# Performance work log

Hardware: AMD Instinct MI355X
Metric: run time of the kernel (lower is better)

Reference implementation:

```python
import jax, jax.numpy as jnp
import numpy as np
from jax import lax

WIN = 9  # NCC window per axis (default [9]*3)

# 3x3x3 edge/shape kernels, shape [O=1, I=1, 3, 3, 3]
_LAP = np.zeros((3, 3, 3), np.float32)
_LAP[1, 1, 1] = 6.0
_LAP[0, 1, 1] = _LAP[2, 1, 1] = -1.0
_LAP[1, 0, 1] = _LAP[1, 2, 1] = -1.0
_LAP[1, 1, 0] = _LAP[1, 1, 2] = -1.0
LAP_K = jnp.asarray(_LAP)[None, None]

_row = np.array([[-1.0, 0.0, 1.0], [-2.0, 0.0, 2.0], [-1.0, 0.0, 1.0]], np.float32)
SOBEL_X = jnp.asarray(np.stack([_row, _row, _row], axis=0))[None, None]
_plane = np.array([[-1.0, -2.0, -1.0], [-1.0, -2.0, -1.0], [-1.0, -2.0, -1.0]], np.float32)
SOBEL_Y = jnp.asarray(np.stack([_plane, np.zeros((3, 3), np.float32), -_plane], axis=0))[None, None]
_zp = np.array([[-1.0, -1.0, -1.0], [0.0, 0.0, 0.0], [1.0, 1.0, 1.0]], np.float32)
SOBEL_Z = jnp.asarray(np.stack([_zp, 2.0 * _zp, _zp], axis=0))[None, None]


def conv3d(x, k, pad):
    # x: [N,C,D,H,W], k: [O,I,kd,kh,kw]
    return lax.conv_general_dilated(x, k, (1, 1, 1), [(pad, pad)] * 3)


def box_sum(x, win=WIN):
    # Separable all-ones box filter == dense ones conv (same math, fewer FLOPs)
    pad = win // 2
    for axis in range(3):
        kshape = [1, 1, 1, 1, 1]
        kshape[2 + axis] = win
        k = jnp.ones(kshape, x.dtype)
        padding = [(pad, pad) if a == axis else (0, 0) for a in range(3)]
        x = lax.conv_general_dilated(x, k, (1, 1, 1), padding)
    return x


def ncc_vxm(Ii, Ji, win=WIN):
    win_size = float(win ** 3)
    I2, J2, IJ = Ii * Ii, Ji * Ji, Ii * Ji
    I_sum = box_sum(Ii, win)
    J_sum = box_sum(Ji, win)
    I2_sum = box_sum(I2, win)
    J2_sum = box_sum(J2, win)
    IJ_sum = box_sum(IJ, win)
    u_I = I_sum / win_size
    u_J = J_sum / win_size
    cross = IJ_sum - u_J * I_sum - u_I * J_sum + u_I * u_J * win_size
    I_var = I2_sum - 2.0 * u_I * I_sum + u_I * u_I * win_size
    J_var = J2_sum - 2.0 * u_J * J_sum + u_J * u_J * win_size
    cc = cross * cross / (I_var * J_var + 1e-5)
    return -jnp.mean(cc)


def edge_detection(v):
    return conv3d(v, LAP_K, pad=1)


def shape_detection(v):
    gx = conv3d(v, SOBEL_X, pad=1)
    gy = conv3d(v, SOBEL_Y, pad=1)
    gz = conv3d(v, SOBEL_Z, pad=1)
    return jnp.sqrt(gx * gx + gy * gy + gz * gz)


def setup_inputs() -> dict:
    key = jax.random.key(0)
    k1, k2 = jax.random.split(key)
    shape = (1, 1, 160, 192, 160)
    y_true = jax.random.uniform(k1, shape, dtype=jnp.float32)
    y_pred = jax.random.uniform(k2, shape, dtype=jnp.float32)
    return {"y_true": y_true, "y_pred": y_pred}


def reference(y_true, y_pred):
    loss_orig = ncc_vxm(y_true, y_pred)
    loss_edge = ncc_vxm(edge_detection(y_true), edge_detection(y_pred))
    loss_shape = ncc_vxm(shape_detection(y_true), shape_detection(y_pred))
    return 0.8 * loss_orig + 0.1 * loss_edge + 0.1 * loss_shape
```

## Files before the change

### kernel.cpp

```cpp
#include <hip/hip_runtime.h>
#include <hip/hip_fp16.h>
#include <math.h>

#define DD 160
#define HHH 192
#define WWW 160
constexpr int HW = HHH * WWW;
constexpr int NV = DD * HHH * WWW;
constexpr int W4 = WWW / 4;
constexpr int HC = 4;
constexpr int DC = 4;
constexpr int SC = 5;

constexpr int NB_WH  = (W4 * DD * (HHH / HC)) / 256;
constexpr int NB_SO  = (W4 * HHH * (DD / SC)) / 256;
constexpr int NB_LAP = (NV / 4) / 256;
constexpr int NB_DCC = (W4 * HHH * (DD / DC)) / 256;

__device__ __forceinline__ float4 ldg4(const float* __restrict__ p, int idx, bool ok) {
    float4 z = make_float4(0.f, 0.f, 0.f, 0.f);
    return ok ? *(const float4*)(p + idx) : z;
}

__device__ __forceinline__ void st_h4(__half* __restrict__ t, int idx,
                                      float s0, float s1, float s2, float s3) {
    union { __half2 h2[2]; uint2 u; } pk;
    pk.h2[0] = __floats2half2_rn(s0, s1);
    pk.h2[1] = __floats2half2_rn(s2, s3);
    *(uint2*)(t + idx) = pk.u;
}

__device__ __forceinline__ void ld_h4(const __half* __restrict__ t, int idx, float o[4]) {
    union { __half2 h2[2]; uint2 u; } pk;
    pk.u = *(const uint2*)(t + idx);
    o[0] = __low2float(pk.h2[0]); o[1] = __high2float(pk.h2[0]);
    o[2] = __low2float(pk.h2[1]); o[3] = __high2float(pk.h2[1]);
}

__device__ __forceinline__ void lap_body(int t, const float* __restrict__ a,
                                         const float* __restrict__ b,
                                         __half* __restrict__ oa, __half* __restrict__ ob) {
    int w = (t % W4) * 4;
    int h = (t / W4) % HHH;
    int d = t / (W4 * HHH);
    int idx = (d * HHH + h) * WWW + w;
    bool dok0 = d > 0, dok1 = d < DD - 1, hok0 = h > 0, hok1 = h < HHH - 1;
#pragma unroll
    for (int s = 0; s < 2; s++) {
        const float* p = s ? b : a;
        __half* o = s ? ob : oa;
        float4 c = *(const float4*)(p + idx);
        float m1 = (w > 0) ? p[idx - 1] : 0.f;
        float p4 = (w + 4 < WWW) ? p[idx + 4] : 0.f;
        float4 dm = ldg4(p, idx - HW, dok0);
        float4 dp = ldg4(p, idx + HW, dok1);
        float4 hm = ldg4(p, idx - WWW, hok0);
        float4 hp = ldg4(p, idx + WWW, hok1);
        st_h4(o, idx,
              6.f * c.x - (m1 + c.y + dm.x + dp.x + hm.x + hp.x),
              6.f * c.y - (c.x + c.z + dm.y + dp.y + hm.y + hp.y),
              6.f * c.z - (c.y + c.w + dm.z + dp.z + hm.z + hp.z),
              6.f * c.w - (c.z + p4 + dm.w + dp.w + hm.w + hp.w));
    }
}

__device__ __forceinline__ void sobel_slice(const float* __restrict__ p, int s, int h, int w,
                                            float a1[4], float a2[4], float a3[4]) {
#pragma unroll
    for (int k = 0; k < 4; k++) { a1[k] = 0.f; a2[k] = 0.f; a3[k] = 0.f; }
#pragma unroll
    for (int kh = -1; kh <= 1; kh++) {
        int h2 = h + kh;
        if ((unsigned)h2 < (unsigned)HHH) {
            int rb = (s * HHH + h2) * WWW + w;
            float4 cen = *(const float4*)(p + rb);
            float xm = (w > 0) ? p[rb - 1] : 0.f;
            float xp = (w + 4 < WWW) ? p[rb + 4] : 0.f;
            float xv[6] = {xm, cen.x, cen.y, cen.z, cen.w, xp};
            float smh = (kh == 0) ? 2.f : 1.f;
            float grh = (float)kh;
#pragma unroll
            for (int k = 0; k < 4; k++) {
                float gw = xv[k + 2] - xv[k];
                float pw = xv[k] + xv[k + 1] + xv[k + 2];
                float sw = pw + xv[k + 1];
                a1[k] += smh * gw;
                a2[k] += sw;
                a3[k] += grh * pw;
            }
        }
    }
}

__device__ __forceinline__ void sobel_body(int t, const float* __restrict__ a,
                                           const float* __restrict__ b,
                                           __half* __restrict__ oa, __half* __restrict__ ob) {
    int w = (t % W4) * 4;
    int h = (t / W4) % HHH;
    int c = t / (W4 * HHH);
    int d0 = c * SC;

    float A1[2][3][4], A2[2][3][4], A3[2][3][4];
#pragma unroll
    for (int r = 0; r < 2; r++)
#pragma unroll
        for (int j = 0; j < 3; j++)
#pragma unroll
            for (int k = 0; k < 4; k++) { A1[r][j][k] = 0.f; A2[r][j][k] = 0.f; A3[r][j][k] = 0.f; }

#pragma unroll
    for (int i = 0; i < SC + 2; i++) {
        int s = d0 - 1 + i;
#pragma unroll
        for (int r = 0; r < 2; r++)
#pragma unroll
            for (int k = 0; k < 4; k++) {
                A1[r][0][k] = A1[r][1][k]; A2[r][0][k] = A2[r][1][k]; A3[r][0][k] = A3[r][1][k];
                A1[r][1][k] = A1[r][2][k]; A2[r][1][k] = A2[r][2][k]; A3[r][1][k] = A3[r][2][k];
            }
        if (s >= 0 && s < DD) {
            sobel_slice(a, s, h, w, A1[0][2], A2[0][2], A3[0][2]);
            sobel_slice(b, s, h, w, A1[1][2], A2[1][2], A3[1][2]);
        } else {
#pragma unroll
            for (int r = 0; r < 2; r++)
#pragma unroll
                for (int k = 0; k < 4; k++) { A1[r][2][k] = 0.f; A2[r][2][k] = 0.f; A3[r][2][k] = 0.f; }
        }
        if (i >= 2) {
            int d = s - 1;
            int idx = (d * HHH + h) * WWW + w;
            float va[4], vb[4];
#pragma unroll
            for (int k = 0; k < 4; k++) {
                float gx = A1[0][0][k] + A1[0][1][k] + A1[0][2][k];
                float gy = A2[0][2][k] - A2[0][0][k];
                float gz = A3[0][0][k] + 2.f * A3[0][1][k] + A3[0][2][k];
                va[k] = sqrtf(gx * gx + gy * gy + gz * gz);
                gx = A1[1][0][k] + A1[1][1][k] + A1[1][2][k];
                gy = A2[1][2][k] - A2[1][0][k];
                gz = A3[1][0][k] + 2.f * A3[1][1][k] + A3[1][2][k];
                vb[k] = sqrtf(gx * gx + gy * gy + gz * gz);
            }
            st_h4(oa, idx, va[0], va[1], va[2], va[3]);
            st_h4(ob, idx, vb[0], vb[1], vb[2], vb[3]);
        }
    }
}

__device__ __forceinline__ void q5_from(const float x[12], const float y[12], float q[5][4]) {
    float s0 = 0, s1 = 0, s2 = 0, s3 = 0, s4 = 0;
#pragma unroll
    for (int j = 0; j < 9; j++) {
        s0 += x[j]; s1 += y[j];
        s2 += x[j] * x[j]; s3 += y[j] * y[j]; s4 += x[j] * y[j];
    }
    q[0][0] = s0; q[1][0] = s1; q[2][0] = s2; q[3][0] = s3; q[4][0] = s4;
#pragma unroll
    for (int k = 1; k < 4; k++) {
        q[0][k] = q[0][k - 1] + x[k + 8] - x[k - 1];
        q[1][k] = q[1][k - 1] + y[k + 8] - y[k - 1];
        q[2][k] = q[2][k - 1] + x[k + 8] * x[k + 8] - x[k - 1] * x[k - 1];
        q[3][k] = q[3][k - 1] + y[k + 8] * y[k + 8] - y[k - 1] * y[k - 1];
        q[4][k] = q[4][k - 1] + x[k + 8] * y[k + 8] - x[k - 1] * y[k - 1];
    }
}

__device__ __forceinline__ void ld12(const float* __restrict__ p, int rowbase, int w, float x[12]) {
    bool lo = (w >= 4);
    bool hi = (w + 7 < WWW);
    float4 x0 = ldg4(p, rowbase + w - 4, lo);
    float4 x1 = *(const float4*)(p + rowbase + w);
    float4 x2 = ldg4(p, rowbase + w + 4, hi);
    x[0] = x0.x; x[1] = x0.y; x[2] = x0.z; x[3] = x0.w;
    x[4] = x1.x; x[5] = x1.y; x[6] = x1.z; x[7] = x1.w;
    x[8] = x2.x; x[9] = x2.y; x[10] = x2.z; x[11] = x2.w;
}

__device__ __forceinline__ void ld12(const __half* __restrict__ p, int rowbase, int w, float x[12]) {
    bool lo = (w >= 4);
    bool hi = (w + 7 < WWW);
    union { __half2 h2[2]; uint2 u; } u0, u1, u2;
    uint2 z = make_uint2(0, 0);
    u0.u = lo ? *(const uint2*)(p + rowbase + w - 4) : z;
    u1.u = *(const uint2*)(p + rowbase + w);
    u2.u = hi ? *(const uint2*)(p + rowbase + w + 4) : z;
    x[0] = __low2float(u0.h2[0]); x[1] = __high2float(u0.h2[0]);
    x[2] = __low2float(u0.h2[1]); x[3] = __high2float(u0.h2[1]);
    x[4] = __low2float(u1.h2[0]); x[5] = __high2float(u1.h2[0]);
    x[6] = __low2float(u1.h2[1]); x[7] = __high2float(u1.h2[1]);
    x[8] = __low2float(u2.h2[0]); x[9] = __high2float(u2.h2[0]);
    x[10] = __low2float(u2.h2[1]); x[11] = __high2float(u2.h2[1]);
}

template <typename T>
__device__ __forceinline__ void rowq5(const T* __restrict__ a, const T* __restrict__ b,
                                      int rowbase, int w, float q[5][4]) {
    float x[12], y[12];
    ld12(a, rowbase, w, x);
    ld12(b, rowbase, w, y);
    q5_from(x, y, q);
}

template <typename T>
__device__ void whsum_body(int t, const T* __restrict__ a, const T* __restrict__ b,
                           __half* __restrict__ t0, __half* __restrict__ t1,
                           __half* __restrict__ t2, __half* __restrict__ t3,
                           __half* __restrict__ t4) {
    int w = (t % W4) * 4;
    int d = (t / W4) % DD;
    int c = t / (W4 * DD);
    int h0 = c * HC;

    float S[5][4] = {{0}};
    for (int j = 0; j < 9; j++) {
        int r = h0 - 4 + j;
        if ((unsigned)r < (unsigned)HHH) {
            float q[5][4];
            rowq5(a, b, (d * HHH + r) * WWW, w, q);
#pragma unroll
            for (int qq = 0; qq < 5; qq++)
#pragma unroll
                for (int k = 0; k < 4; k++) S[qq][k] += q[qq][k];
        }
    }
    {
        int idx = (d * HHH + h0) * WWW + w;
        st_h4(t0, idx, S[0][0], S[0][1], S[0][2], S[0][3]);
        st_h4(t1, idx, S[1][0], S[1][1], S[1][2], S[1][3]);
        st_h4(t2, idx, S[2][0], S[2][1], S[2][2], S[2][3]);
        st_h4(t3, idx, S[3][0], S[3][1], S[3][2], S[3][3]);
        st_h4(t4, idx, S[4][0], S[4][1], S[4][2], S[4][3]);
    }
    for (int h = h0 + 1; h < h0 + HC; h++) {
        int rin = h + 4, rout = h - 5;
        if (rin < HHH) {
            float q[5][4];
            rowq5(a, b, (d * HHH + rin) * WWW, w, q);
#pragma unroll
            for (int qq = 0; qq < 5; qq++)
#pragma unroll
                for (int k = 0; k < 4; k++) S[qq][k] += q[qq][k];
        }
        if (rout >= 0) {
            float q[5][4];
            rowq5(a, b, (d * HHH + rout) * WWW, w, q);
#pragma unroll
            for (int qq = 0; qq < 5; qq++)
#pragma unroll
                for (int k = 0; k < 4; k++) S[qq][k] -= q[qq][k];
        }
        int idx = (d * HHH + h) * WWW + w;
        st_h4(t0, idx, S[0][0], S[0][1], S[0][2], S[0][3]);
        st_h4(t1, idx, S[1][0], S[1][1], S[1][2], S[1][3]);
        st_h4(t2, idx, S[2][0], S[2][1], S[2][2], S[2][3]);
        st_h4(t3, idx, S[3][0], S[3][1], S[3][2], S[3][3]);
        st_h4(t4, idx, S[4][0], S[4][1], S[4][2], S[4][3]);
    }
}

__device__ __forceinline__ float cc1(float s0, float s1, float s2, float s3, float s4) {
    const float wsz = 729.0f;
    const float inv = 1.0f / 729.0f;
    float uI = s0 * inv;
    float uJ = s1 * inv;
    float cross = s4 - uJ * s0 - uI * s1 + uI * uJ * wsz;
    float Iv = s2 - 2.0f * uI * s0 + uI * uI * wsz;
    float Jv = s3 - 2.0f * uJ * s1 + uJ * uJ * wsz;
    return cross * cross / (Iv * Jv + 1e-5f);
}

__device__ void dcc_body(int t, const __half* __restrict__ t0, const __half* __restrict__ t1,
                         const __half* __restrict__ t2, const __half* __restrict__ t3,
                         const __half* __restrict__ t4, double* __restrict__ acc, int pair) {
    int w = (t % W4) * 4;
    int h = (t / W4) % HHH;
    int c = t / (W4 * HHH);
    int d0 = c * DC;

    float S[5][4] = {{0}};
    for (int j = 0; j < 9; j++) {
        int r = d0 - 4 + j;
        if ((unsigned)r < (unsigned)DD) {
            int idx = (r * HHH + h) * WWW + w;
            float v[5][4];
            ld_h4(t0, idx, v[0]); ld_h4(t1, idx, v[1]); ld_h4(t2, idx, v[2]);
            ld_h4(t3, idx, v[3]); ld_h4(t4, idx, v[4]);
#pragma unroll
            for (int q = 0; q < 5; q++)
#pragma unroll
                for (int k = 0; k < 4; k++) S[q][k] += v[q][k];
        }
    }
    float local = 0.f;
#pragma unroll
    for (int k = 0; k < 4; k++) local += cc1(S[0][k], S[1][k], S[2][k], S[3][k], S[4][k]);
#pragma unroll
    for (int d = 1; d < DC; d++) {
        int rin = d0 + d + 4, rout = d0 + d - 5;
        if (rin < DD) {
            int idx = (rin * HHH + h) * WWW + w;
            float v[5][4];
            ld_h4(t0, idx, v[0]); ld_h4(t1, idx, v[1]); ld_h4(t2, idx, v[2]);
            ld_h4(t3, idx, v[3]); ld_h4(t4, idx, v[4]);
#pragma unroll
            for (int q = 0; q < 5; q++)
#pragma unroll
                for (int k = 0; k < 4; k++) S[q][k] += v[q][k];
        }
        if (rout >= 0) {
            int idx = (rout * HHH + h) * WWW + w;
            float v[5][4];
            ld_h4(t0, idx, v[0]); ld_h4(t1, idx, v[1]); ld_h4(t2, idx, v[2]);
            ld_h4(t3, idx, v[3]); ld_h4(t4, idx, v[4]);
#pragma unroll
            for (int q = 0; q < 5; q++)
#pragma unroll
                for (int k = 0; k < 4; k++) S[q][k] -= v[q][k];
        }
#pragma unroll
        for (int k = 0; k < 4; k++) local += cc1(S[0][k], S[1][k], S[2][k], S[3][k], S[4][k]);
    }

    for (int off = 32; off > 0; off >>= 1) local += __shfl_down(local, off);
    __shared__ float wsum_[4];
    if ((threadIdx.x & 63) == 0) wsum_[threadIdx.x >> 6] = local;
    __syncthreads();
    if (threadIdx.x == 0) {
        float s = wsum_[0] + wsum_[1] + wsum_[2] + wsum_[3];
        atomicAdd(&acc[pair], (double)s);
    }
}

__global__ void stage1(const float* __restrict__ yt, const float* __restrict__ yp,
                       __half* __restrict__ e1a, __half* __restrict__ e1b,
                       __half* __restrict__ e2a, __half* __restrict__ e2b,
                       __half* __restrict__ ta0, __half* __restrict__ ta1,
                       __half* __restrict__ ta2, __half* __restrict__ ta3,
                       __half* __restrict__ ta4, double* __restrict__ acc) {
    int b = blockIdx.x;
    if (b < NB_WH) {
        whsum_body<float>(b * 256 + threadIdx.x, yt, yp, ta0, ta1, ta2, ta3, ta4);
    } else if (b < NB_WH + NB_SO) {
        sobel_body((b - NB_WH) * 256 + threadIdx.x, yt, yp, e2a, e2b);
    } else if (b < NB_WH + NB_SO + NB_LAP) {
        lap_body((b - NB_WH - NB_SO) * 256 + threadIdx.x, yt, yp, e1a, e1b);
    } else {
        if (threadIdx.x < 3) acc[threadIdx.x] = 0.0;
    }
}

__global__ void stage23(const __half* __restrict__ ea, const __half* __restrict__ eb,
                        __half* __restrict__ o0, __half* __restrict__ o1,
                        __half* __restrict__ o2, __half* __restrict__ o3,
                        __half* __restrict__ o4,
                        const __half* __restrict__ i0, const __half* __restrict__ i1,
                        const __half* __restrict__ i2, const __half* __restrict__ i3,
                        const __half* __restrict__ i4, double* __restrict__ acc, int pair) {
    int b = blockIdx.x;
    if (b < NB_WH) {
        whsum_body<__half>(b * 256 + threadIdx.x, ea, eb, o0, o1, o2, o3, o4);
    } else {
        dcc_body((b - NB_WH) * 256 + threadIdx.x, i0, i1, i2, i3, i4, acc, pair);
    }
}

__global__ void dcc_k(const __half* __restrict__ t0, const __half* __restrict__ t1,
                      const __half* __restrict__ t2, const __half* __restrict__ t3,
                      const __half* __restrict__ t4, double* __restrict__ acc, int pair) {
    dcc_body(blockIdx.x * 256 + threadIdx.x, t0, t1, t2, t3, t4, acc, pair);
}

__global__ void finalize_k(const double* __restrict__ acc, float* __restrict__ out) {
    if (threadIdx.x == 0) {
        double v = 0.8 * acc[0] + 0.1 * acc[1] + 0.1 * acc[2];
        out[0] = (float)(-v / (double)NV);
    }
}

extern "C" void kernel_launch(void* const* d_in, const int* in_sizes, int n_in,
                              void* d_out, int out_size, void* d_ws, size_t ws_size,
                              hipStream_t stream) {
    const float* yt = (const float*)d_in[0];
    const float* yp = (const float*)d_in[1];
    float* out = (float*)d_out;

    double* acc = (double*)d_ws;
    __half* base = (__half*)((char*)d_ws + 256);
    __half* e1a = base + 0 * (size_t)NV;
    __half* e1b = base + 1 * (size_t)NV;
    __half* e2a = base + 2 * (size_t)NV;
    __half* e2b = base + 3 * (size_t)NV;
    __half* tA = base + 4 * (size_t)NV;
    __half* tB = base + 9 * (size_t)NV;

    dim3 blk(256);

    hipLaunchKernelGGL(stage1, dim3(NB_WH + NB_SO + NB_LAP + 1), blk, 0, stream,
                       yt, yp, e1a, e1b, e2a, e2b,
                       tA, tA + NV, tA + 2 * (size_t)NV, tA + 3 * (size_t)NV, tA + 4 * (size_t)NV,
                       acc);
    hipLaunchKernelGGL(stage23, dim3(NB_WH + NB_DCC), blk, 0, stream,
                       e1a, e1b,
                       tB, tB + NV, tB + 2 * (size_t)NV, tB + 3 * (size_t)NV, tB + 4 * (size_t)NV,
                       tA, tA + NV, tA + 2 * (size_t)NV, tA + 3 * (size_t)NV, tA + 4 * (size_t)NV,
                       acc, 0);
    hipLaunchKernelGGL(stage23, dim3(NB_WH + NB_DCC), blk, 0, stream,
                       e2a, e2b,
                       tA, tA + NV, tA + 2 * (size_t)NV, tA + 3 * (size_t)NV, tA + 4 * (size_t)NV,
                       tB, tB + NV, tB + 2 * (size_t)NV, tB + 3 * (size_t)NV, tB + 4 * (size_t)NV,
                       acc, 1);
    hipLaunchKernelGGL(dcc_k, dim3(NB_DCC), blk, 0, stream,
                       tA, tA + NV, tA + 2 * (size_t)NV, tA + 3 * (size_t)NV, tA + 4 * (size_t)NV,
                       acc, 2);

    hipLaunchKernelGGL(finalize_k, dim3(1), dim3(1), 0, stream, acc, out);
}
```

Baseline: 382.3 us.

## Merge edge and shape NCC passes into two wider launches with extra buffer

When the workspace has room for a third set of five half-precision box-sum buffers, the edge and shape WH-sum passes now run in one launch alongside the original-image D-pass. Both remaining D-pass reductions then run together in a second launch. This cuts the launch chain from four kernels to three and gives each launch a larger grid, reducing launch gaps and tail underutilisation. The cost is roughly 5*NV more halfs of workspace. If the workspace is too small it falls back to the old sequence.

Result: no change. 375.2 us (median of 2 runs) (-1.9%).

```diff
diff --git a/kernel.cpp b/kernel.cpp
--- a/kernel.cpp
+++ b/kernel.cpp
@@ -371,6 +371,37 @@
     dcc_body(blockIdx.x * 256 + threadIdx.x, t0, t1, t2, t3, t4, acc, pair);
 }
 
+__global__ void stage2b(const __half* __restrict__ e1a, const __half* __restrict__ e1b,
+                        const __half* __restrict__ e2a, const __half* __restrict__ e2b,
+                        __half* __restrict__ tB, __half* __restrict__ tC,
+                        const __half* __restrict__ tA, double* __restrict__ acc) {
+    int b = blockIdx.x;
+    size_t nv = (size_t)NV;
+    if (b < NB_WH) {
+        whsum_body<__half>(b * 256 + threadIdx.x, e1a, e1b,
+                           tB, tB + nv, tB + 2 * nv, tB + 3 * nv, tB + 4 * nv);
+    } else if (b < 2 * NB_WH) {
+        whsum_body<__half>((b - NB_WH) * 256 + threadIdx.x, e2a, e2b,
+                           tC, tC + nv, tC + 2 * nv, tC + 3 * nv, tC + 4 * nv);
+    } else {
+        dcc_body((b - 2 * NB_WH) * 256 + threadIdx.x,
+                 tA, tA + nv, tA + 2 * nv, tA + 3 * nv, tA + 4 * nv, acc, 0);
+    }
+}
+
+__global__ void stage3b(const __half* __restrict__ tB, const __half* __restrict__ tC,
+                        double* __restrict__ acc) {
+    int b = blockIdx.x;
+    size_t nv = (size_t)NV;
+    if (b < NB_DCC) {
+        dcc_body(b * 256 + threadIdx.x,
+                 tB, tB + nv, tB + 2 * nv, tB + 3 * nv, tB + 4 * nv, acc, 1);
+    } else {
+        dcc_body((b - NB_DCC) * 256 + threadIdx.x,
+                 tC, tC + nv, tC + 2 * nv, tC + 3 * nv, tC + 4 * nv, acc, 2);
+    }
+}
+
 __global__ void finalize_k(const double* __restrict__ acc, float* __restrict__ out) {
     if (threadIdx.x == 0) {
         double v = 0.8 * acc[0] + 0.1 * acc[1] + 0.1 * acc[2];
@@ -387,32 +418,41 @@
 
     double* acc = (double*)d_ws;
     __half* base = (__half*)((char*)d_ws + 256);
-    __half* e1a = base + 0 * (size_t)NV;
-    __half* e1b = base + 1 * (size_t)NV;
-    __half* e2a = base + 2 * (size_t)NV;
-    __half* e2b = base + 3 * (size_t)NV;
-    __half* tA = base + 4 * (size_t)NV;
-    __half* tB = base + 9 * (size_t)NV;
+    size_t nv = (size_t)NV;
+    __half* e1a = base + 0 * nv;
+    __half* e1b = base + 1 * nv;
+    __half* e2a = base + 2 * nv;
+    __half* e2b = base + 3 * nv;
+    __half* tA = base + 4 * nv;
+    __half* tB = base + 9 * nv;
+    __half* tC = base + 14 * nv;
+
+    bool wide = ws_size >= 256 + 19 * nv * sizeof(__half);
 
     dim3 blk(256);
 
     hipLaunchKernelGGL(stage1, dim3(NB_WH + NB_SO + NB_LAP + 1), blk, 0, stream,
                        yt, yp, e1a, e1b, e2a, e2b,
-                       tA, tA + NV, tA + 2 * (size_t)NV, tA + 3 * (size_t)NV, tA + 4 * (size_t)NV,
-                       acc);
-    hipLaunchKernelGGL(stage23, dim3(NB_WH + NB_DCC), blk, 0, stream,
-                       e1a, e1b,
-                       tB, tB + NV, tB + 2 * (size_t)NV, tB + 3 * (size_t)NV, tB + 4 * (size_t)NV,
-                       tA, tA + NV, tA + 2 * (size_t)NV, tA + 3 * (size_t)NV, tA + 4 * (size_t)NV,
-                       acc, 0);
-    hipLaunchKernelGGL(stage23, dim3(NB_WH + NB_DCC), blk, 0, stream,
-                       e2a, e2b,
-                       tA, tA + NV, tA + 2 * (size_t)NV, tA + 3 * (size_t)NV, tA + 4 * (size_t)NV,
-                       tB, tB + NV, tB + 2 * (size_t)NV, tB + 3 * (size_t)NV, tB + 4 * (size_t)NV,
-                       acc, 1);
-    hipLaunchKernelGGL(dcc_k, dim3(NB_DCC), blk, 0, stream,
-                       tA, tA + NV, tA + 2 * (size_t)NV, tA + 3 * (size_t)NV, tA + 4 * (size_t)NV,
-                       acc, 2);
+                       tA, tA + nv, tA + 2 * nv, tA + 3 * nv, tA + 4 * nv, acc);
+
+    if (wide) {
+        hipLaunchKernelGGL(stage2b, dim3(2 * NB_WH + NB_DCC), blk, 0, stream,
+                           e1a, e1b, e2a, e2b, tB, tC, tA, acc);
+        hipLaunchKernelGGL(stage3b, dim3(2 * NB_DCC), blk, 0, stream, tB, tC, acc);
+    } else {
+        hipLaunchKernelGGL(stage23, dim3(NB_WH + NB_DCC), blk, 0, stream,
+                           e1a, e1b,
+                           tB, tB + nv, tB + 2 * nv, tB + 3 * nv, tB + 4 * nv,
+                           tA, tA + nv, tA + 2 * nv, tA + 3 * nv, tA + 4 * nv,
+                           acc, 0);
+        hipLaunchKernelGGL(stage23, dim3(NB_WH + NB_DCC), blk, 0, stream,
+                           e2a, e2b,
+                           tA, tA + nv, tA + 2 * nv, tA + 3 * nv, tA + 4 * nv,
+                           tB, tB + nv, tB + 2 * nv, tB + 3 * nv, tB + 4 * nv,
+                           acc, 1);
+        hipLaunchKernelGGL(dcc_k, dim3(NB_DCC), blk, 0, stream,
+                           tA, tA + nv, tA + 2 * nv, tA + 3 * nv, tA + 4 * nv, acc, 2);
+    }
 
     hipLaunchKernelGGL(finalize_k, dim3(1), dim3(1), 0, stream, acc, out);
 }
```
